# Kernel optimization log

Measured on AMD Instinct MI355X. Metric: run time of the kernel, lower is better.

## Reference

```python
import jax, jax.numpy as jnp
import numpy as np

N = 100_000   # nodes
E = 3_200_000  # edges (avg degree 32)


def setup_inputs() -> dict:
    key = jax.random.key(0)
    ks = jax.random.split(key, 8)
    x = jax.random.normal(ks[0], (N, 4), dtype=jnp.float32)
    edge_index = jax.random.randint(ks[1], (2, E), 0, N, dtype=jnp.int64)
    # GCNConv weights: lin(in,out,bias=False) then bias added post-aggregation
    W1 = jax.random.normal(ks[2], (4, 16), dtype=jnp.float32) * 0.5
    b1 = jax.random.normal(ks[3], (16,), dtype=jnp.float32) * 0.1
    W2 = jax.random.normal(ks[4], (16, 32), dtype=jnp.float32) * 0.25
    b2 = jax.random.normal(ks[5], (32,), dtype=jnp.float32) * 0.1
    Wfc = jax.random.normal(ks[6], (32, 4), dtype=jnp.float32) * 0.2
    bfc = jax.random.normal(ks[7], (4,), dtype=jnp.float32) * 0.1
    return {"x": x, "edge_index": edge_index, "W1": W1, "b1": b1,
            "W2": W2, "b2": b2, "Wfc": Wfc, "bfc": bfc}


def _gcn_conv(x, W, b, src, dst, norm):
    # h_j = x_j @ W ; out_i = sum_{j->i} norm_ij * h_j ; + bias
    n = x.shape[0]
    h = x @ W
    msg = h[src] * norm[:, None]              # [E+N, out]
    out = jax.ops.segment_sum(msg, dst, num_segments=n)
    return out + b


def reference(x, edge_index, W1, b1, W2, b2, Wfc, bfc):
    n = x.shape[0]
    loops = jnp.arange(n, dtype=edge_index.dtype)
    src = jnp.concatenate([edge_index[0], loops])  # PyG: row = source j
    dst = jnp.concatenate([edge_index[1], loops])  # col = target i
    # symmetric normalization with self-loops (PyG gcn_norm default)
    deg = jax.ops.segment_sum(jnp.ones(dst.shape[0], x.dtype), dst, num_segments=n)
    dinv = jnp.where(deg > 0, jax.lax.rsqrt(deg), jnp.zeros_like(deg))
    norm = dinv[src] * dinv[dst]

    h = jax.nn.relu(_gcn_conv(x, W1, b1, src, dst, norm))
    h = jax.nn.relu(_gcn_conv(h, W2, b2, src, dst, norm))
    return h @ Wfc + bfc
```

## Files before the change

### kernel.cpp

```cpp
#include <hip/hip_runtime.h>
#include <hip/hip_bf16.h>
#include <hip/hip_fp16.h>


#define NBUCK 1024
#define TILE  8192
#define EPT   8
#define BSH   7
#define CAP   5120

__global__ void k_zero(int* __restrict__ gcur) {
    gcur[blockIdx.x * 512 + threadIdx.x] = 0;
}

__global__ __launch_bounds__(1024)
void k_bucket(const int* __restrict__ src, const int* __restrict__ dst,
              int* __restrict__ gcur, int* __restrict__ colbkt, int E) {
    __shared__ int hist[NBUCK];
    __shared__ int wcur[NBUCK];
    int t = threadIdx.x;
    int tb = blockIdx.x * TILE;
    int cntT = min(TILE, E - tb);

    hist[t] = 0;
    __syncthreads();

    int sv[EPT], dv[EPT];
    #pragma unroll
    for (int j = 0; j < EPT; j++) {
        int i = t + j * 1024;
        bool ok = i < cntT;
        sv[j] = ok ? src[tb + i] : 0;
        dv[j] = ok ? dst[tb + i] : 0;
        if (ok) atomicAdd(&hist[dv[j] >> BSH], 1);
    }
    __syncthreads();

    {
        int c = hist[t];
        wcur[t] = (c > 0) ? atomicAdd(&gcur[t], c) : 0;
    }
    __syncthreads();

    #pragma unroll
    for (int j = 0; j < EPT; j++) {
        int i = t + j * 1024;
        if (i < cntT) {
            int b = dv[j] >> BSH;
            int pos = atomicAdd(&wcur[b], 1);
            if (pos < CAP)
                colbkt[(size_t)b * CAP + pos] =
                    sv[j] | ((dv[j] & ((1 << BSH) - 1)) << 17);
        }
    }
}

__global__ __launch_bounds__(512)
void k_sortpre(const int* __restrict__ gcur, int* __restrict__ colbkt,
               const float* __restrict__ x, float* __restrict__ dinv,
               __half* __restrict__ g1h, int* __restrict__ rowbeg,
               int* __restrict__ rowlen, int n) {
    __shared__ int recbuf[CAP];
    __shared__ int hist[128];
    __shared__ int offs[128];
    __shared__ int cur[128];
    __shared__ int wtot;
    int t = threadIdx.x, b = blockIdx.x;
    int nb = min(gcur[b], CAP);
    int* row = colbkt + (size_t)b * CAP;
    if (t < 128) hist[t] = 0;
    __syncthreads();
    for (int e = t; e < nb; e += 512) {
        int rec = __builtin_nontemporal_load(row + e);
        recbuf[e] = rec;
        atomicAdd(&hist[(rec >> 17) & 127], 1);
    }
    __syncthreads();
    int h = (t < 128) ? hist[t] : 0;
    int lane = t & 63;
    int incl = h;
    #pragma unroll
    for (int off = 1; off < 64; off <<= 1) {
        int v = __shfl_up(incl, off);
        if (lane >= off) incl += v;
    }
    if (t == 63) wtot = incl;
    __syncthreads();
    if (t < 128) {
        int incl2 = incl + ((t >= 64) ? wtot : 0);
        offs[t] = incl2;
        cur[t] = incl2 - h;
    }
    __syncthreads();
    for (int e = t; e < nb; e += 512) {
        int rec = recbuf[e];
        int dl = (rec >> 17) & 127;
        int p = atomicAdd(&cur[dl], 1);
        row[p] = rec;
    }
    if (t < 128) {
        int node = (b << BSH) + t;
        if (node < n) {
            int len = hist[t];
            rowlen[node] = len;
            rowbeg[node] = b * CAP + (offs[t] - len);
            float di = rsqrtf((float)len + 1.0f);
            dinv[node] = di;
            float4 xv = *reinterpret_cast<const float4*>(x + (size_t)node * 4);
            union { __half2 h2[2]; uint2 u2; } pk;
            pk.h2[0] = __floats2half2_rn(di * xv.x, di * xv.y);
            pk.h2[1] = __floats2half2_rn(di * xv.z, di * xv.w);
            *reinterpret_cast<uint2*>(g1h + (size_t)node * 4) = pk.u2;
        }
    }
}

__device__ __forceinline__ void add_g1(float& a0, float& a1, float& a2, float& a3,
                                       uint2 u) {
    float2 f0 = __half22float2(*reinterpret_cast<const __half2*>(&u.x));
    float2 f1 = __half22float2(*reinterpret_cast<const __half2*>(&u.y));
    a0 += f0.x; a1 += f0.y; a2 += f1.x; a3 += f1.y;
}

__global__ __launch_bounds__(256)
void k_gather1(const int* __restrict__ rowbeg, const int* __restrict__ rowlen,
               const int* __restrict__ colbkt, const __half* __restrict__ g1h,
               const float* __restrict__ dinv, const float* __restrict__ W1,
               const float* __restrict__ b1, __half* __restrict__ g2h, int n) {
    __shared__ float w[64];
    __shared__ float bb[16];
    if (threadIdx.x < 64) w[threadIdx.x] = W1[threadIdx.x];
    if (threadIdx.x >= 64 && threadIdx.x < 80) bb[threadIdx.x - 64] = b1[threadIdx.x - 64];
    __syncthreads();
    int gt = blockIdx.x * 256 + threadIdx.x;
    int i = gt >> 2;
    int lane = gt & 3;
    if (i >= n) return;
    int len = rowlen[i];
    const int* row = colbkt + rowbeg[i];
    const uint2* g1v = reinterpret_cast<const uint2*>(g1h);
    float a0 = 0.f, a1 = 0.f, a2 = 0.f, a3 = 0.f;
    if (lane == 0)
        add_g1(a0, a1, a2, a3, g1v[i]);
    int e = lane;
    for (; e + 12 < len; e += 16) {
        int r0 = __builtin_nontemporal_load(row + e);
        int r1 = __builtin_nontemporal_load(row + e + 4);
        int r2 = __builtin_nontemporal_load(row + e + 8);
        int r3 = __builtin_nontemporal_load(row + e + 12);
        uint2 u0 = g1v[r0 & 0x1FFFF];
        uint2 u1 = g1v[r1 & 0x1FFFF];
        uint2 u2 = g1v[r2 & 0x1FFFF];
        uint2 u3 = g1v[r3 & 0x1FFFF];
        add_g1(a0, a1, a2, a3, u0);
        add_g1(a0, a1, a2, a3, u1);
        add_g1(a0, a1, a2, a3, u2);
        add_g1(a0, a1, a2, a3, u3);
    }
    for (; e < len; e += 4) {
        int rec = __builtin_nontemporal_load(row + e);
        add_g1(a0, a1, a2, a3, g1v[rec & 0x1FFFF]);
    }
    a0 += __shfl_xor(a0, 1); a1 += __shfl_xor(a1, 1);
    a2 += __shfl_xor(a2, 1); a3 += __shfl_xor(a3, 1);
    a0 += __shfl_xor(a0, 2); a1 += __shfl_xor(a1, 2);
    a2 += __shfl_xor(a2, 2); a3 += __shfl_xor(a3, 2);
    if (lane != 0) return;
    float di = dinv[i];
    a0 *= di; a1 *= di; a2 *= di; a3 *= di;
    union { __half2 h2[8]; uint4 u4[2]; } pk;
    #pragma unroll
    for (int c = 0; c < 8; c++) {
        int f0 = 2 * c, f1 = 2 * c + 1;
        float r0 = di * fmaxf(a0*w[f0] + a1*w[16+f0] + a2*w[32+f0] + a3*w[48+f0] + bb[f0], 0.f);
        float r1 = di * fmaxf(a0*w[f1] + a1*w[16+f1] + a2*w[32+f1] + a3*w[48+f1] + bb[f1], 0.f);
        pk.h2[c] = __floats2half2_rn(r0, r1);
    }
    uint4* o = reinterpret_cast<uint4*>(g2h + (size_t)i * 16);
    o[0] = pk.u4[0];
    o[1] = pk.u4[1];
}

__device__ __forceinline__ void add_g2(float* acc, uint4 a, uint4 b) {
    const __half2* pa = reinterpret_cast<const __half2*>(&a);
    const __half2* pb = reinterpret_cast<const __half2*>(&b);
    #pragma unroll
    for (int j = 0; j < 4; j++) {
        float2 f = __half22float2(pa[j]);
        acc[2*j] += f.x; acc[2*j+1] += f.y;
    }
    #pragma unroll
    for (int j = 0; j < 4; j++) {
        float2 f = __half22float2(pb[j]);
        acc[8+2*j] += f.x; acc[8+2*j+1] += f.y;
    }
}

__global__ __launch_bounds__(256)
void k_gather2(const int* __restrict__ rowbeg, const int* __restrict__ rowlen,
               const int* __restrict__ colbkt, const __half* __restrict__ g2h,
               const float* __restrict__ dinv, const float* __restrict__ W2,
               const float* __restrict__ b2, const float* __restrict__ Wfc,
               const float* __restrict__ bfc, float* __restrict__ out, int n) {
    __shared__ float w2[512];
    __shared__ float wf[128];
    __shared__ float b2s[32];
    __shared__ float bfs[4];
    for (int j = threadIdx.x; j < 512; j += blockDim.x) w2[j] = W2[j];
    if (threadIdx.x < 128) wf[threadIdx.x] = Wfc[threadIdx.x];
    if (threadIdx.x >= 128 && threadIdx.x < 160) b2s[threadIdx.x - 128] = b2[threadIdx.x - 128];
    if (threadIdx.x >= 160 && threadIdx.x < 164) bfs[threadIdx.x - 160] = bfc[threadIdx.x - 160];
    __syncthreads();

    int gt = blockIdx.x * 256 + threadIdx.x;
    int i = gt >> 3;
    int lane = gt & 7;
    if (i >= n) return;
    int len = rowlen[i];
    const int* row = colbkt + rowbeg[i];
    const uint4* g2v = reinterpret_cast<const uint4*>(g2h);

    float acc[16];
    #pragma unroll
    for (int k = 0; k < 16; k++) acc[k] = 0.f;
    if (lane == 0)
        add_g2(acc, g2v[(size_t)i * 2], g2v[(size_t)i * 2 + 1]);
    int e = lane;
    for (; e + 24 < len; e += 32) {
        int r0 = __builtin_nontemporal_load(row + e);
        int r1 = __builtin_nontemporal_load(row + e + 8);
        int r2 = __builtin_nontemporal_load(row + e + 16);
        int r3 = __builtin_nontemporal_load(row + e + 24);
        size_t s0 = (size_t)(r0 & 0x1FFFF) * 2;
        size_t s1 = (size_t)(r1 & 0x1FFFF) * 2;
        size_t s2 = (size_t)(r2 & 0x1FFFF) * 2;
        size_t s3 = (size_t)(r3 & 0x1FFFF) * 2;
        uint4 a0 = g2v[s0], c0 = g2v[s0 + 1];
        uint4 a1 = g2v[s1], c1 = g2v[s1 + 1];
        uint4 a2 = g2v[s2], c2 = g2v[s2 + 1];
        uint4 a3 = g2v[s3], c3 = g2v[s3 + 1];
        add_g2(acc, a0, c0);
        add_g2(acc, a1, c1);
        add_g2(acc, a2, c2);
        add_g2(acc, a3, c3);
    }
    for (; e < len; e += 8) {
        int rec = __builtin_nontemporal_load(row + e);
        size_t s = (size_t)(rec & 0x1FFFF) * 2;
        add_g2(acc, g2v[s], g2v[s + 1]);
    }
    #pragma unroll
    for (int k = 0; k < 16; k++) acc[k] += __shfl_xor(acc[k], 1);
    #pragma unroll
    for (int k = 0; k < 16; k++) acc[k] += __shfl_xor(acc[k], 2);
    #pragma unroll
    for (int k = 0; k < 16; k++) acc[k] += __shfl_xor(acc[k], 4);

    float di = dinv[i];
    #pragma unroll
    for (int k = 0; k < 16; k++) acc[k] *= di;

    float o0 = (lane == 0) ? bfs[0] : 0.f;
    float o1 = (lane == 0) ? bfs[1] : 0.f;
    float o2 = (lane == 0) ? bfs[2] : 0.f;
    float o3 = (lane == 0) ? bfs[3] : 0.f;
    int fbase = lane * 4;
    #pragma unroll
    for (int fo = 0; fo < 4; fo++) {
        int f = fbase + fo;
        float h = b2s[f];
        #pragma unroll
        for (int k = 0; k < 16; k++) h += acc[k] * w2[k * 32 + f];
        h = fmaxf(h, 0.0f);
        o0 += h * wf[f * 4 + 0];
        o1 += h * wf[f * 4 + 1];
        o2 += h * wf[f * 4 + 2];
        o3 += h * wf[f * 4 + 3];
    }
    o0 += __shfl_xor(o0, 1); o1 += __shfl_xor(o1, 1);
    o2 += __shfl_xor(o2, 1); o3 += __shfl_xor(o3, 1);
    o0 += __shfl_xor(o0, 2); o1 += __shfl_xor(o1, 2);
    o2 += __shfl_xor(o2, 2); o3 += __shfl_xor(o3, 2);
    o0 += __shfl_xor(o0, 4); o1 += __shfl_xor(o1, 4);
    o2 += __shfl_xor(o2, 4); o3 += __shfl_xor(o3, 4);
    if (lane != 0) return;
    float4 r; r.x = o0; r.y = o1; r.z = o2; r.w = o3;
    *reinterpret_cast<float4*>(out + (size_t)i * 4) = r;
}

extern "C" void kernel_launch(void* const* d_in, const int* in_sizes, int n_in,
                              void* d_out, int out_size, void* d_ws, size_t ws_size,
                              hipStream_t stream) {
    const float* x   = (const float*)d_in[0];
    const int*   ei  = (const int*)d_in[1];
    const float* W1  = (const float*)d_in[2];
    const float* b1  = (const float*)d_in[3];
    const float* W2  = (const float*)d_in[4];
    const float* b2  = (const float*)d_in[5];
    const float* Wfc = (const float*)d_in[6];
    const float* bfc = (const float*)d_in[7];
    float* out = (float*)d_out;

    const int n = in_sizes[0] / 4;
    const int E = in_sizes[1] / 2;
    const int* src = ei;
    const int* dst = ei + E;

    char* p = (char*)d_ws;
    int*    gcur   = (int*)p;           p += (size_t)NBUCK * 4;
    int*    colbkt = (int*)p;           p += (size_t)NBUCK * CAP * 4;
    int*    rowbeg = (int*)p;           p += (size_t)n * 4;
    int*    rowlen = (int*)p;           p += (size_t)n * 4;
    float*  dinv   = (float*)p;         p += (size_t)n * 4;
    __half* g1h    = (__half*)p;        p += (size_t)n * 8;
    __half* g2h    = (__half*)p;        p += (size_t)n * 32;

    const int NBu = (n + 127) >> BSH;
    const int gT  = (E + TILE - 1) / TILE;
    const int gN4 = ((size_t)n * 4 + 255) / 256;
    const int gN8 = ((size_t)n * 8 + 255) / 256;

    k_zero   <<<NBUCK / 512, 512, 0, stream>>>(gcur);
    k_bucket <<<gT,  1024, 0, stream>>>(src, dst, gcur, colbkt, E);
    k_sortpre<<<NBu, 512, 0, stream>>>(gcur, colbkt, x, dinv, g1h, rowbeg, rowlen, n);
    k_gather1<<<gN4, 256, 0, stream>>>(rowbeg, rowlen, colbkt, g1h, dinv, W1, b1, g2h, n);
    k_gather2<<<gN8, 256, 0, stream>>>(rowbeg, rowlen, colbkt, g2h, dinv,
                                       W2, b2, Wfc, bfc, out, n);
}
```

Measured before the change: 123.1 us.

## Fuse all GCN stages into one persistent cooperative kernel with grid syncs

Replaces the five launches (zero, bucket, sort/prep, gather1, gather2) with a single cooperative kernel of 512 blocks by 512 threads. Stages are separated by grid.sync(), and a shared-memory union is reused across stages. Bucketing uses smaller tiles with more edges per thread, and the other stages are grid-strided. The aim is to remove launch gaps and tail effects between kernels. The cost is grid-wide barriers, a fixed grid size that may limit occupancy, and register pressure from putting every stage in one kernel. The old multi-kernel path remains as a fallback if the cooperative launch fails.

```diff
diff --git a/kernel.cpp b/kernel.cpp
--- a/kernel.cpp
+++ b/kernel.cpp
@@ -1,13 +1,291 @@
 #include <hip/hip_runtime.h>
 #include <hip/hip_bf16.h>
 #include <hip/hip_fp16.h>
+#include <hip/hip_cooperative_groups.h>
+
+namespace cg = cooperative_groups;
 
 
 #define NBUCK 1024
-#define TILE  8192
-#define EPT   8
 #define BSH   7
 #define CAP   5120
+#define NTHR  512
+#define NBLK  512
+#define TILE  6144
+#define EPT   12
+
+union SharedU {
+    struct { int hist[NBUCK]; int wcur[NBUCK]; } bkt;
+    struct { int recbuf[CAP]; int hist[128]; int offs[128]; int cur[128]; int wtot; } srt;
+    struct { float w[64]; float bb[16]; } g1;
+    struct { float w2[512]; float wf[128]; float b2s[32]; float bfs[4]; } g2;
+};
+
+__device__ __forceinline__ void add_g1(float& a0, float& a1, float& a2, float& a3,
+                                       uint2 u) {
+    float2 f0 = __half22float2(*reinterpret_cast<const __half2*>(&u.x));
+    float2 f1 = __half22float2(*reinterpret_cast<const __half2*>(&u.y));
+    a0 += f0.x; a1 += f0.y; a2 += f1.x; a3 += f1.y;
+}
+
+__device__ __forceinline__ void add_g2(float* acc, uint4 a, uint4 b) {
+    const __half2* pa = reinterpret_cast<const __half2*>(&a);
+    const __half2* pb = reinterpret_cast<const __half2*>(&b);
+    #pragma unroll
+    for (int j = 0; j < 4; j++) {
+        float2 f = __half22float2(pa[j]);
+        acc[2*j] += f.x; acc[2*j+1] += f.y;
+    }
+    #pragma unroll
+    for (int j = 0; j < 4; j++) {
+        float2 f = __half22float2(pb[j]);
+        acc[8+2*j] += f.x; acc[8+2*j+1] += f.y;
+    }
+}
+
+__global__ __launch_bounds__(NTHR, 4)
+void k_fused(const int* __restrict__ src, const int* __restrict__ dst,
+             const float* __restrict__ x,
+             const float* __restrict__ W1, const float* __restrict__ b1,
+             const float* __restrict__ W2, const float* __restrict__ b2,
+             const float* __restrict__ Wfc, const float* __restrict__ bfc,
+             float* __restrict__ out,
+             int* __restrict__ gcur, int* __restrict__ colbkt,
+             int* __restrict__ rowbeg, int* __restrict__ rowlen,
+             float* __restrict__ dinv, __half* __restrict__ g1h,
+             __half* __restrict__ g2h, int n, int E) {
+    __shared__ SharedU sh;
+    cg::grid_group grid = cg::this_grid();
+    int t = threadIdx.x;
+    int gt0 = blockIdx.x * NTHR + t;
+    int stride = gridDim.x * NTHR;
+
+    if (gt0 < NBUCK) gcur[gt0] = 0;
+    grid.sync();
+
+    int nT = (E + TILE - 1) / TILE;
+    for (int tile = blockIdx.x; tile < nT; tile += gridDim.x) {
+        int tb = tile * TILE;
+        int cntT = min(TILE, E - tb);
+        sh.bkt.hist[t] = 0; sh.bkt.hist[t + 512] = 0;
+        __syncthreads();
+        int sv[EPT], dv[EPT];
+        #pragma unroll
+        for (int j = 0; j < EPT; j++) {
+            int i = t + j * NTHR;
+            bool ok = i < cntT;
+            sv[j] = ok ? src[tb + i] : 0;
+            dv[j] = ok ? dst[tb + i] : 0;
+            if (ok) atomicAdd(&sh.bkt.hist[dv[j] >> BSH], 1);
+        }
+        __syncthreads();
+        #pragma unroll
+        for (int j = 0; j < 2; j++) {
+            int b = t + j * 512;
+            int c = sh.bkt.hist[b];
+            sh.bkt.wcur[b] = (c > 0) ? atomicAdd(&gcur[b], c) : 0;
+        }
+        __syncthreads();
+        #pragma unroll
+        for (int j = 0; j < EPT; j++) {
+            int i = t + j * NTHR;
+            if (i < cntT) {
+                int b = dv[j] >> BSH;
+                int pos = atomicAdd(&sh.bkt.wcur[b], 1);
+                if (pos < CAP)
+                    colbkt[(size_t)b * CAP + pos] =
+                        sv[j] | ((dv[j] & ((1 << BSH) - 1)) << 17);
+            }
+        }
+        __syncthreads();
+    }
+    grid.sync();
+
+    int NBu = (n + 127) >> BSH;
+    for (int b = blockIdx.x; b < NBu; b += gridDim.x) {
+        int nb = min(gcur[b], CAP);
+        int* row = colbkt + (size_t)b * CAP;
+        if (t < 128) sh.srt.hist[t] = 0;
+        __syncthreads();
+        for (int e = t; e < nb; e += NTHR) {
+            int rec = __builtin_nontemporal_load(row + e);
+            sh.srt.recbuf[e] = rec;
+            atomicAdd(&sh.srt.hist[(rec >> 17) & 127], 1);
+        }
+        __syncthreads();
+        int h = (t < 128) ? sh.srt.hist[t] : 0;
+        int lane = t & 63;
+        int incl = h;
+        #pragma unroll
+        for (int off = 1; off < 64; off <<= 1) {
+            int v = __shfl_up(incl, off);
+            if (lane >= off) incl += v;
+        }
+        if (t == 63) sh.srt.wtot = incl;
+        __syncthreads();
+        if (t < 128) {
+            int incl2 = incl + ((t >= 64) ? sh.srt.wtot : 0);
+            sh.srt.offs[t] = incl2;
+            sh.srt.cur[t] = incl2 - h;
+        }
+        __syncthreads();
+        for (int e = t; e < nb; e += NTHR) {
+            int rec = sh.srt.recbuf[e];
+            int dl = (rec >> 17) & 127;
+            int p = atomicAdd(&sh.srt.cur[dl], 1);
+            row[p] = rec;
+        }
+        if (t < 128) {
+            int node = (b << BSH) + t;
+            if (node < n) {
+                int len = sh.srt.hist[t];
+                rowlen[node] = len;
+                rowbeg[node] = b * CAP + (sh.srt.offs[t] - len);
+                float di = rsqrtf((float)len + 1.0f);
+                dinv[node] = di;
+                float4 xv = *reinterpret_cast<const float4*>(x + (size_t)node * 4);
+                union { __half2 h2[2]; uint2 u2; } pk;
+                pk.h2[0] = __floats2half2_rn(di * xv.x, di * xv.y);
+                pk.h2[1] = __floats2half2_rn(di * xv.z, di * xv.w);
+                *reinterpret_cast<uint2*>(g1h + (size_t)node * 4) = pk.u2;
+            }
+        }
+        __syncthreads();
+    }
+    grid.sync();
+
+    if (t < 64) sh.g1.w[t] = W1[t];
+    if (t >= 64 && t < 80) sh.g1.bb[t - 64] = b1[t - 64];
+    __syncthreads();
+    for (int gt = gt0; gt < n * 4; gt += stride) {
+        int i = gt >> 2;
+        int lane = gt & 3;
+        int len = rowlen[i];
+        const int* row = colbkt + rowbeg[i];
+        const uint2* g1v = reinterpret_cast<const uint2*>(g1h);
+        float a0 = 0.f, a1 = 0.f, a2 = 0.f, a3 = 0.f;
+        if (lane == 0)
+            add_g1(a0, a1, a2, a3, g1v[i]);
+        int e = lane;
+        for (; e + 12 < len; e += 16) {
+            int r0 = __builtin_nontemporal_load(row + e);
+            int r1 = __builtin_nontemporal_load(row + e + 4);
+            int r2 = __builtin_nontemporal_load(row + e + 8);
+            int r3 = __builtin_nontemporal_load(row + e + 12);
+            uint2 u0 = g1v[r0 & 0x1FFFF];
+            uint2 u1 = g1v[r1 & 0x1FFFF];
+            uint2 u2 = g1v[r2 & 0x1FFFF];
+            uint2 u3 = g1v[r3 & 0x1FFFF];
+            add_g1(a0, a1, a2, a3, u0);
+            add_g1(a0, a1, a2, a3, u1);
+            add_g1(a0, a1, a2, a3, u2);
+            add_g1(a0, a1, a2, a3, u3);
+        }
+        for (; e < len; e += 4) {
+            int rec = __builtin_nontemporal_load(row + e);
+            add_g1(a0, a1, a2, a3, g1v[rec & 0x1FFFF]);
+        }
+        a0 += __shfl_xor(a0, 1); a1 += __shfl_xor(a1, 1);
+        a2 += __shfl_xor(a2, 1); a3 += __shfl_xor(a3, 1);
+        a0 += __shfl_xor(a0, 2); a1 += __shfl_xor(a1, 2);
+        a2 += __shfl_xor(a2, 2); a3 += __shfl_xor(a3, 2);
+        if (lane == 0) {
+            float di = dinv[i];
+            a0 *= di; a1 *= di; a2 *= di; a3 *= di;
+            union { __half2 h2[8]; uint4 u4[2]; } pk;
+            #pragma unroll
+            for (int c = 0; c < 8; c++) {
+                int f0 = 2 * c, f1 = 2 * c + 1;
+                float r0 = di * fmaxf(a0*sh.g1.w[f0] + a1*sh.g1.w[16+f0] + a2*sh.g1.w[32+f0] + a3*sh.g1.w[48+f0] + sh.g1.bb[f0], 0.f);
+                float r1 = di * fmaxf(a0*sh.g1.w[f1] + a1*sh.g1.w[16+f1] + a2*sh.g1.w[32+f1] + a3*sh.g1.w[48+f1] + sh.g1.bb[f1], 0.f);
+                pk.h2[c] = __floats2half2_rn(r0, r1);
+            }
+            uint4* o = reinterpret_cast<uint4*>(g2h + (size_t)i * 16);
+            o[0] = pk.u4[0];
+            o[1] = pk.u4[1];
+        }
+    }
+    grid.sync();
+
+    for (int j = t; j < 512; j += NTHR) sh.g2.w2[j] = W2[j];
+    if (t < 128) sh.g2.wf[t] = Wfc[t];
+    if (t >= 128 && t < 160) sh.g2.b2s[t - 128] = b2[t - 128];
+    if (t >= 160 && t < 164) sh.g2.bfs[t - 160] = bfc[t - 160];
+    __syncthreads();
+    for (int gt = gt0; gt < n * 8; gt += stride) {
+        int i = gt >> 3;
+        int lane = gt & 7;
+        int len = rowlen[i];
+        const int* row = colbkt + rowbeg[i];
+        const uint4* g2v = reinterpret_cast<const uint4*>(g2h);
+        float acc[16];
+        #pragma unroll
+        for (int k = 0; k < 16; k++) acc[k] = 0.f;
+        if (lane == 0)
+            add_g2(acc, g2v[(size_t)i * 2], g2v[(size_t)i * 2 + 1]);
+        int e = lane;
+        for (; e + 24 < len; e += 32) {
+            int r0 = __builtin_nontemporal_load(row + e);
+            int r1 = __builtin_nontemporal_load(row + e + 8);
+            int r2 = __builtin_nontemporal_load(row + e + 16);
+            int r3 = __builtin_nontemporal_load(row + e + 24);
+            size_t s0 = (size_t)(r0 & 0x1FFFF) * 2;
+            size_t s1 = (size_t)(r1 & 0x1FFFF) * 2;
+            size_t s2 = (size_t)(r2 & 0x1FFFF) * 2;
+            size_t s3 = (size_t)(r3 & 0x1FFFF) * 2;
+            uint4 a0 = g2v[s0], c0 = g2v[s0 + 1];
+            uint4 a1 = g2v[s1], c1 = g2v[s1 + 1];
+            uint4 a2 = g2v[s2], c2 = g2v[s2 + 1];
+            uint4 a3 = g2v[s3], c3 = g2v[s3 + 1];
+            add_g2(acc, a0, c0);
+            add_g2(acc, a1, c1);
+            add_g2(acc, a2, c2);
+            add_g2(acc, a3, c3);
+        }
+        for (; e < len; e += 8) {
+            int rec = __builtin_nontemporal_load(row + e);
+            size_t s = (size_t)(rec & 0x1FFFF) * 2;
+            add_g2(acc, g2v[s], g2v[s + 1]);
+        }
+        #pragma unroll
+        for (int k = 0; k < 16; k++) acc[k] += __shfl_xor(acc[k], 1);
+        #pragma unroll
+        for (int k = 0; k < 16; k++) acc[k] += __shfl_xor(acc[k], 2);
+        #pragma unroll
+        for (int k = 0; k < 16; k++) acc[k] += __shfl_xor(acc[k], 4);
+        float di = dinv[i];
+        #pragma unroll
+        for (int k = 0; k < 16; k++) acc[k] *= di;
+        float o0 = (lane == 0) ? sh.g2.bfs[0] : 0.f;
+        float o1 = (lane == 0) ? sh.g2.bfs[1] : 0.f;
+        float o2 = (lane == 0) ? sh.g2.bfs[2] : 0.f;
+        float o3 = (lane == 0) ? sh.g2.bfs[3] : 0.f;
+        int fbase = lane * 4;
+        #pragma unroll
+        for (int fo = 0; fo < 4; fo++) {
+            int f = fbase + fo;
+            float h = sh.g2.b2s[f];
+            #pragma unroll
+            for (int k = 0; k < 16; k++) h += acc[k] * sh.g2.w2[k * 32 + f];
+            h = fmaxf(h, 0.0f);
+            o0 += h * sh.g2.wf[f * 4 + 0];
+            o1 += h * sh.g2.wf[f * 4 + 1];
+            o2 += h * sh.g2.wf[f * 4 + 2];
+            o3 += h * sh.g2.wf[f * 4 + 3];
+        }
+        o0 += __shfl_xor(o0, 1); o1 += __shfl_xor(o1, 1);
+        o2 += __shfl_xor(o2, 1); o3 += __shfl_xor(o3, 1);
+        o0 += __shfl_xor(o0, 2); o1 += __shfl_xor(o1, 2);
+        o2 += __shfl_xor(o2, 2); o3 += __shfl_xor(o3, 2);
+        o0 += __shfl_xor(o0, 4); o1 += __shfl_xor(o1, 4);
+        o2 += __shfl_xor(o2, 4); o3 += __shfl_xor(o3, 4);
+        if (lane == 0) {
+            float4 r; r.x = o0; r.y = o1; r.z = o2; r.w = o3;
+            *reinterpret_cast<float4*>(out + (size_t)i * 4) = r;
+        }
+    }
+}
+
 
 __global__ void k_zero(int* __restrict__ gcur) {
     gcur[blockIdx.x * 512 + threadIdx.x] = 0;
@@ -19,15 +297,14 @@
     __shared__ int hist[NBUCK];
     __shared__ int wcur[NBUCK];
     int t = threadIdx.x;
-    int tb = blockIdx.x * TILE;
-    int cntT = min(TILE, E - tb);
-
+    const int BT = 8192;
+    int tb = blockIdx.x * BT;
+    int cntT = min(BT, E - tb);
     hist[t] = 0;
     __syncthreads();
-
-    int sv[EPT], dv[EPT];
-    #pragma unroll
-    for (int j = 0; j < EPT; j++) {
+    int sv[8], dv[8];
+    #pragma unroll
+    for (int j = 0; j < 8; j++) {
         int i = t + j * 1024;
         bool ok = i < cntT;
         sv[j] = ok ? src[tb + i] : 0;
@@ -35,15 +312,13 @@
         if (ok) atomicAdd(&hist[dv[j] >> BSH], 1);
     }
     __syncthreads();
-
     {
         int c = hist[t];
         wcur[t] = (c > 0) ? atomicAdd(&gcur[t], c) : 0;
     }
     __syncthreads();
-
-    #pragma unroll
-    for (int j = 0; j < EPT; j++) {
+    #pragma unroll
+    for (int j = 0; j < 8; j++) {
         int i = t + j * 1024;
         if (i < cntT) {
             int b = dv[j] >> BSH;
@@ -113,13 +388,6 @@
             *reinterpret_cast<uint2*>(g1h + (size_t)node * 4) = pk.u2;
         }
     }
-}
-
-__device__ __forceinline__ void add_g1(float& a0, float& a1, float& a2, float& a3,
-                                       uint2 u) {
-    float2 f0 = __half22float2(*reinterpret_cast<const __half2*>(&u.x));
-    float2 f1 = __half22float2(*reinterpret_cast<const __half2*>(&u.y));
-    a0 += f0.x; a1 += f0.y; a2 += f1.x; a3 += f1.y;
 }
 
 __global__ __launch_bounds__(256)
@@ -181,21 +449,6 @@
     o[1] = pk.u4[1];
 }
 
-__device__ __forceinline__ void add_g2(float* acc, uint4 a, uint4 b) {
-    const __half2* pa = reinterpret_cast<const __half2*>(&a);
-    const __half2* pb = reinterpret_cast<const __half2*>(&b);
-    #pragma unroll
-    for (int j = 0; j < 4; j++) {
-        float2 f = __half22float2(pa[j]);
-        acc[2*j] += f.x; acc[2*j+1] += f.y;
-    }
-    #pragma unroll
-    for (int j = 0; j < 4; j++) {
-        float2 f = __half22float2(pb[j]);
-        acc[8+2*j] += f.x; acc[8+2*j+1] += f.y;
-    }
-}
-
 __global__ __launch_bounds__(256)
 void k_gather2(const int* __restrict__ rowbeg, const int* __restrict__ rowlen,
                const int* __restrict__ colbkt, const __half* __restrict__ g2h,
@@ -211,7 +464,6 @@
     if (threadIdx.x >= 128 && threadIdx.x < 160) b2s[threadIdx.x - 128] = b2[threadIdx.x - 128];
     if (threadIdx.x >= 160 && threadIdx.x < 164) bfs[threadIdx.x - 160] = bfc[threadIdx.x - 160];
     __syncthreads();
-
     int gt = blockIdx.x * 256 + threadIdx.x;
     int i = gt >> 3;
     int lane = gt & 7;
@@ -219,7 +471,6 @@
     int len = rowlen[i];
     const int* row = colbkt + rowbeg[i];
     const uint4* g2v = reinterpret_cast<const uint4*>(g2h);
-
     float acc[16];
     #pragma unroll
     for (int k = 0; k < 16; k++) acc[k] = 0.f;
@@ -255,11 +506,9 @@
     for (int k = 0; k < 16; k++) acc[k] += __shfl_xor(acc[k], 2);
     #pragma unroll
     for (int k = 0; k < 16; k++) acc[k] += __shfl_xor(acc[k], 4);
-
     float di = dinv[i];
     #pragma unroll
     for (int k = 0; k < 16; k++) acc[k] *= di;
-
     float o0 = (lane == 0) ? bfs[0] : 0.f;
     float o1 = (lane == 0) ? bfs[1] : 0.f;
     float o2 = (lane == 0) ? bfs[2] : 0.f;
@@ -291,6 +540,8 @@
 extern "C" void kernel_launch(void* const* d_in, const int* in_sizes, int n_in,
                               void* d_out, int out_size, void* d_ws, size_t ws_size,
                               hipStream_t stream) {
+    const int* src_p   = (const int*)d_in[0 + 1];
+    (void)src_p;
     const float* x   = (const float*)d_in[0];
     const int*   ei  = (const int*)d_in[1];
     const float* W1  = (const float*)d_in[2];
@@ -301,8 +552,8 @@
     const float* bfc = (const float*)d_in[7];
     float* out = (float*)d_out;
 
-    const int n = in_sizes[0] / 4;
-    const int E = in_sizes[1] / 2;
+    int n = in_sizes[0] / 4;
+    int E = in_sizes[1] / 2;
     const int* src = ei;
     const int* dst = ei + E;
 
@@ -315,13 +566,21 @@
     __half* g1h    = (__half*)p;        p += (size_t)n * 8;
     __half* g2h    = (__half*)p;        p += (size_t)n * 32;
 
+    void* args[] = { (void*)&src, (void*)&dst, (void*)&x,
+                     (void*)&W1, (void*)&b1, (void*)&W2, (void*)&b2,
+                     (void*)&Wfc, (void*)&bfc, (void*)&out,
+                     (void*)&gcur, (void*)&colbkt, (void*)&rowbeg, (void*)&rowlen,
+                     (void*)&dinv, (void*)&g1h, (void*)&g2h, (void*)&n, (void*)&E };
+    hipError_t err = hipLaunchCooperativeKernel((void*)k_fused, dim3(NBLK), dim3(NTHR),
+                                                args, 0, stream);
+    if (err == hipSuccess) return;
+
     const int NBu = (n + 127) >> BSH;
-    const int gT  = (E + TILE - 1) / TILE;
+    const int gTf = (E + 8191) / 8192;
     const int gN4 = ((size_t)n * 4 + 255) / 256;
     const int gN8 = ((size_t)n * 8 + 255) / 256;
-
     k_zero   <<<NBUCK / 512, 512, 0, stream>>>(gcur);
-    k_bucket <<<gT,  1024, 0, stream>>>(src, dst, gcur, colbkt, E);
+    k_bucket <<<gTf, 1024, 0, stream>>>(src, dst, gcur, colbkt, E);
     k_sortpre<<<NBu, 512, 0, stream>>>(gcur, colbkt, x, dinv, g1h, rowbeg, rowlen, n);
     k_gather1<<<gN4, 256, 0, stream>>>(rowbeg, rowlen, colbkt, g1h, dinv, W1, b1, g2h, n);
     k_gather2<<<gN8, 256, 0, stream>>>(rowbeg, rowlen, colbkt, g2h, dinv,
```

Result: slower. 420.4 us (+241.4%).
